# Performance work log

Measured on AMD Instinct MI355X. Metric: run time of the kernel, lower is better.

The kernel has to match this reference:

```python
import jax, jax.numpy as jnp
import numpy as np

N_NODES = 100000
N_EDGES = 3200000
N_GRAPHS = 512


def setup_inputs() -> dict:
    key = jax.random.key(0)
    k1, k2, k3, k4, k5 = jax.random.split(key, 5)
    x = jax.random.normal(k1, (N_NODES, 5), dtype=jnp.float32)
    edge_index = jax.random.randint(k2, (2, N_EDGES), 0, N_NODES, dtype=jnp.int64)
    batch = jnp.sort(jax.random.randint(k3, (N_NODES,), 0, N_GRAPHS, dtype=jnp.int64))
    W1 = jax.random.normal(k4, (5, 16), dtype=jnp.float32) * (1.0 / np.sqrt(5.0))
    b1 = jnp.zeros((16,), dtype=jnp.float32)
    W2 = jax.random.normal(k5, (16, 16), dtype=jnp.float32) * 0.25
    b2 = jnp.zeros((16,), dtype=jnp.float32)
    return {"x": x, "edge_index": edge_index, "batch": batch,
            "W1": W1, "b1": b1, "W2": W2, "b2": b2}


def _gcn_conv(x, src, dst, norm, W, b, n_nodes):
    # PyG GCNConv: h = X W; out_i = sum_{j->i} norm_ij * h_j + b
    h = x @ W                                   # [N, out]
    msgs = h[src] * norm[:, None]               # gather + scale  [E_tot, out]
    out = jax.ops.segment_sum(msgs, dst, num_segments=n_nodes)
    return out + b


def reference(x, edge_index, batch, W1, b1, W2, b2):
    n = x.shape[0]
    # add self-loops (GCNConv default)
    loops = jnp.arange(n, dtype=edge_index.dtype)
    src = jnp.concatenate([edge_index[0], loops])
    dst = jnp.concatenate([edge_index[1], loops])
    # symmetric normalization: deg computed on destination nodes
    deg = jax.ops.segment_sum(jnp.ones_like(src, dtype=x.dtype), dst, num_segments=n)
    dinv = jnp.where(deg > 0, jax.lax.rsqrt(deg), 0.0)
    norm = dinv[src] * dinv[dst]                # [E_tot]

    h = jax.nn.relu(_gcn_conv(x, src, dst, norm, W1, b1, n))
    h = jax.nn.relu(_gcn_conv(h, src, dst, norm, W2, b2, n))

    # global mean pool over graphs in the batch
    sums = jax.ops.segment_sum(h, batch, num_segments=N_GRAPHS)
    cnts = jax.ops.segment_sum(jnp.ones((n,), dtype=h.dtype), batch, num_segments=N_GRAPHS)
    return sums / jnp.maximum(cnts, 1.0)[:, None]
```

## Files before the change

kernel.cpp:

```cpp
#include <hip/hip_runtime.h>

#define N_NODES  100000
#define N_EDGES  3200000
#define N_GRAPHS 512
#define F_IN     5
#define F_HID    16

#define PBLK   512
#define CHUNK  4096
#define NBLK   ((N_EDGES + CHUNK - 1) / CHUNK)
#define BKT_NODES 256
#define NBKT ((N_NODES + BKT_NODES - 1) / BKT_NODES)
#define HPAD   512
#define CAP    10240
#define PN     64
#define NPB    ((N_NODES + PN - 1) / PN)


__device__ inline unsigned short f2bf(float f) {
    unsigned u = __float_as_uint(f);
    return (unsigned short)((u + 0x7fffu + ((u >> 16) & 1u)) >> 16);
}
__device__ inline float bf2f(unsigned short h) {
    return __uint_as_float(((unsigned)h) << 16);
}
__device__ inline void unpack16(uint4 r0, uint4 r1, float* f) {
    f[0]  = bf2f((unsigned short)r0.x); f[1]  = bf2f((unsigned short)(r0.x >> 16));
    f[2]  = bf2f((unsigned short)r0.y); f[3]  = bf2f((unsigned short)(r0.y >> 16));
    f[4]  = bf2f((unsigned short)r0.z); f[5]  = bf2f((unsigned short)(r0.z >> 16));
    f[6]  = bf2f((unsigned short)r0.w); f[7]  = bf2f((unsigned short)(r0.w >> 16));
    f[8]  = bf2f((unsigned short)r1.x); f[9]  = bf2f((unsigned short)(r1.x >> 16));
    f[10] = bf2f((unsigned short)r1.y); f[11] = bf2f((unsigned short)(r1.y >> 16));
    f[12] = bf2f((unsigned short)r1.z); f[13] = bf2f((unsigned short)(r1.z >> 16));
    f[14] = bf2f((unsigned short)r1.w); f[15] = bf2f((unsigned short)(r1.w >> 16));
}

template <int NW>
__device__ inline int block_incl_scan(int v, int t, int* wsum) {
    int lane = t & 63, wave = t >> 6;
    int x = v;
#pragma unroll
    for (int o = 1; o < 64; o <<= 1) {
        int y = __shfl_up(x, o, 64);
        if (lane >= o) x += y;
    }
    if (lane == 63) wsum[wave] = x;
    __syncthreads();
    if (t < 64) {
        int w = (t < NW) ? wsum[t] : 0;
#pragma unroll
        for (int o = 1; o < NW; o <<= 1) {
            int y = __shfl_up(w, o, 64);
            if (t >= o) w += y;
        }
        if (t < NW) wsum[t] = w;
    }
    __syncthreads();
    return x + (wave ? wsum[wave - 1] : 0);
}


__global__ __launch_bounds__(256) void k_zero(float* __restrict__ out,
                                              float* __restrict__ cnt) {
    int i = blockIdx.x * 256 + threadIdx.x;
    if (i < N_GRAPHS * F_HID) out[i] = 0.0f;
    if (i < N_GRAPHS) cnt[i] = 0.0f;
}

__global__ __launch_bounds__(PBLK) void k_count(const int* __restrict__ dst,
                                                const int* __restrict__ batch,
                                                int* __restrict__ H,
                                                int* __restrict__ Hc,
                                                float* __restrict__ cnt) {
    __shared__ int hist[HPAD];
    __shared__ int bcnt[8];
    __shared__ int g0s;
    int t = threadIdx.x, blk = blockIdx.x;
    int chunk0 = blk * CHUNK;
    int n4 = min(CHUNK, N_EDGES - chunk0) >> 2;
    hist[t] = 0;
    if (t < 8) bcnt[t] = 0;
    if (t == 0 && blk < NBKT) {
        int nb = blk * BKT_NODES;
        g0s = batch[nb < N_NODES ? nb : N_NODES - 1];
    }
    __syncthreads();
    const int4* d4 = (const int4*)(dst + chunk0);
#pragma unroll
    for (int i = 0; i < CHUNK / 4 / PBLK; i++) {
        int k = t + i * PBLK;
        if (k < n4) {
            int4 d = d4[k];
            atomicAdd(&hist[d.x >> 8], 1);
            atomicAdd(&hist[d.y >> 8], 1);
            atomicAdd(&hist[d.z >> 8], 1);
            atomicAdd(&hist[d.w >> 8], 1);
        }
    }
    if (blk < NBKT && t < BKT_NODES) {
        int i2 = blk * BKT_NODES + t;
        if (i2 < N_NODES) {
            int g = batch[i2];
            int l = g - g0s;
            if (l >= 0 && l < 8) atomicAdd(&bcnt[l], 1);
            else atomicAdd(&cnt[g], 1.0f);
        }
    }
    __syncthreads();
    int v = hist[t];
    H[blk * HPAD + t] = v;
    Hc[blk * HPAD + t] = v;
    if (blk < NBKT && t < 8 && bcnt[t] > 0) atomicAdd(&cnt[g0s + t], (float)bcnt[t]);
}

__global__ __launch_bounds__(256) void k_scan(int* __restrict__ H,
                                              int* __restrict__ cnt_b) {
    __shared__ int wsum[8];
    int b = blockIdx.x, t = threadIdx.x;
    int v[4];
    int s = 0;
#pragma unroll
    for (int i = 0; i < 4; i++) {
        int pos = t * 4 + i;
        v[i] = (pos < NBLK) ? H[pos * HPAD + b] : 0;
        s += v[i];
    }
    int incl = block_incl_scan<4>(s, t, wsum);
    int run = incl - s;
#pragma unroll
    for (int i = 0; i < 4; i++) {
        int pos = t * 4 + i;
        if (pos < NBLK) H[pos * HPAD + b] = run;
        run += v[i];
    }
    if (t == 255) cnt_b[b] = incl;
}

__global__ __launch_bounds__(PBLK) void k_scatter(const int* __restrict__ src,
                                                  const int* __restrict__ dst,
                                                  const int* __restrict__ H,
                                                  const int* __restrict__ Hc,
                                                  unsigned* __restrict__ packed) {
    __shared__ int scn[HPAD];
    __shared__ int rnk[HPAD];
    __shared__ int base[HPAD];
    __shared__ int wsum[8];
    __shared__ unsigned pkd[CHUNK];
    __shared__ unsigned short bkt[CHUNK];
    int t = threadIdx.x, blk = blockIdx.x;
    int chunk0 = blk * CHUNK;
    int n = min(CHUNK, N_EDGES - chunk0);
    int n4 = n >> 2;
    base[t] = H[blk * HPAD + t];
    int v = Hc[blk * HPAD + t];
    int incl = block_incl_scan<8>(v, t, wsum);
    int excl = incl - v;
    scn[t] = excl;
    rnk[t] = excl;
    __syncthreads();
    const int4* s4 = (const int4*)(src + chunk0);
    const int4* d4 = (const int4*)(dst + chunk0);
#pragma unroll
    for (int i = 0; i < CHUNK / 4 / PBLK; i++) {
        int k = t + i * PBLK;
        if (k < n4) {
            int4 s = s4[k], d = d4[k];
            int b0 = d.x >> 8, b1 = d.y >> 8, b2 = d.z >> 8, b3 = d.w >> 8;
            int r0 = atomicAdd(&rnk[b0], 1);
            pkd[r0] = ((unsigned)s.x << 8) | (unsigned)(d.x & 255);
            bkt[r0] = (unsigned short)b0;
            int r1 = atomicAdd(&rnk[b1], 1);
            pkd[r1] = ((unsigned)s.y << 8) | (unsigned)(d.y & 255);
            bkt[r1] = (unsigned short)b1;
            int r2 = atomicAdd(&rnk[b2], 1);
            pkd[r2] = ((unsigned)s.z << 8) | (unsigned)(d.z & 255);
            bkt[r2] = (unsigned short)b2;
            int r3 = atomicAdd(&rnk[b3], 1);
            pkd[r3] = ((unsigned)s.w << 8) | (unsigned)(d.w & 255);
            bkt[r3] = (unsigned short)b3;
        }
    }
    __syncthreads();
    for (int p = t; p < n; p += PBLK) {
        int b = bkt[p];
        packed[(size_t)b * CAP + base[b] + (p - scn[b])] = pkd[p];
    }
}

__global__ __launch_bounds__(512) void k_csr(const int* __restrict__ cnt_b,
                                             const unsigned* __restrict__ packed,
                                             const float* __restrict__ x,
                                             const float* __restrict__ W1,
                                             int2* __restrict__ rowbc,
                                             int* __restrict__ col,
                                             float* __restrict__ dinv,
                                             unsigned short* __restrict__ pb) {
    __shared__ int hist[BKT_NODES];
    __shared__ int beg[BKT_NODES];
    __shared__ int rnk2[BKT_NODES];
    __shared__ int wsum[8];
    __shared__ float w1[F_IN * F_HID];
    __shared__ unsigned pkd[CAP];
    __shared__ int tots;
    int b = blockIdx.x, t = threadIdx.x;
    int gbase = b * CAP;
    if (t < BKT_NODES) hist[t] = 0;
    if (t == 0) tots = min(cnt_b[b], CAP);
    if (t >= 512 - F_IN * F_HID) w1[t - (512 - F_IN * F_HID)] = W1[t - (512 - F_IN * F_HID)];
    __syncthreads();
    int tot = tots;
    const unsigned* pk = packed + (size_t)b * CAP;
    for (int k = t; k < tot; k += 512) {
        unsigned u = pk[k];
        pkd[k] = u;
        atomicAdd(&hist[u & 255], 1);
    }
    __syncthreads();
    int v = (t < BKT_NODES) ? hist[t] : 0;
    int incl = block_incl_scan<8>(v, t, wsum);
    if (t < BKT_NODES) { beg[t] = incl - v; rnk2[t] = incl - v; }
    __syncthreads();
    for (int e = t; e < tot; e += 512) {
        unsigned w = pkd[e];
        int r = atomicAdd(&rnk2[w & 255], 1);
        col[gbase + r] = (int)(w >> 8);
    }
    if (t < BKT_NODES) {
        int node = b * BKT_NODES + t;
        if (node < N_NODES) {
            rowbc[node] = make_int2(gbase + beg[t], v);
            float di = rsqrtf((float)(1 + v));
            dinv[node] = di;
            float xi[F_IN];
#pragma unroll
            for (int k = 0; k < F_IN; k++) xi[k] = x[node * F_IN + k];
            unsigned pkk[8];
#pragma unroll
            for (int q = 0; q < 8; q++) {
                float h0 = 0.0f, h1 = 0.0f;
#pragma unroll
                for (int k = 0; k < F_IN; k++) {
                    h0 += xi[k] * w1[k * F_HID + 2 * q];
                    h1 += xi[k] * w1[k * F_HID + 2 * q + 1];
                }
                pkk[q] = (unsigned)f2bf(h0 * di) | ((unsigned)f2bf(h1 * di) << 16);
            }
            uint4* d4 = (uint4*)(pb + (size_t)node * F_HID);
            d4[0] = make_uint4(pkk[0], pkk[1], pkk[2], pkk[3]);
            d4[1] = make_uint4(pkk[4], pkk[5], pkk[6], pkk[7]);
        }
    }
}

__global__ __launch_bounds__(256) void k_pull1(const int2* __restrict__ rowbc,
                                               const int* __restrict__ col,
                                               const unsigned short* __restrict__ pb,
                                               const float* __restrict__ dinv,
                                               const float* __restrict__ W2,
                                               const float* __restrict__ b1,
                                               unsigned short* __restrict__ pb2) {
    __shared__ float w2[F_HID * F_HID];
    __shared__ float b1s[F_HID];
    int t = threadIdx.x;
    w2[t] = W2[t];
    if (t < F_HID) b1s[t] = b1[t];
    __syncthreads();
    int nl = t >> 2, q = t & 3;
    int node = blockIdx.x * PN + nl;
    const uint4* pb16 = (const uint4*)pb;
    float f[F_HID];
#pragma unroll
    for (int c = 0; c < F_HID; c++) f[c] = 0.0f;
    if (node < N_NODES) {
        int2 rc = rowbc[node];
        if (q == 0) unpack16(pb16[2 * node], pb16[2 * node + 1], f);
        for (int i = q; i < rc.y; i += 4) {
            int s = col[rc.x + i];
            uint4 r0 = pb16[2 * s], r1 = pb16[2 * s + 1];
            float g[F_HID];
            unpack16(r0, r1, g);
#pragma unroll
            for (int c = 0; c < F_HID; c++) f[c] += g[c];
        }
    }
#pragma unroll
    for (int c = 0; c < F_HID; c++) {
        f[c] += __shfl_xor(f[c], 1, 64);
        f[c] += __shfl_xor(f[c], 2, 64);
    }
    if (node < N_NODES) {
        float di = dinv[node];
        float h[F_HID];
#pragma unroll
        for (int c = 0; c < F_HID; c++)
            h[c] = fmaxf(di * f[c] + b1s[c], 0.0f);
        float m0 = 0.0f, m1 = 0.0f, m2 = 0.0f, m3 = 0.0f;
#pragma unroll
        for (int c = 0; c < F_HID; c++) {
            float4 wv = *(const float4*)&w2[c * F_HID + 4 * q];
            m0 += h[c] * wv.x; m1 += h[c] * wv.y; m2 += h[c] * wv.z; m3 += h[c] * wv.w;
        }
        unsigned p0 = (unsigned)f2bf(m0 * di) | ((unsigned)f2bf(m1 * di) << 16);
        unsigned p1 = (unsigned)f2bf(m2 * di) | ((unsigned)f2bf(m3 * di) << 16);
        *(uint2*)(pb2 + (size_t)node * F_HID + 4 * q) = make_uint2(p0, p1);
    }
}

__global__ __launch_bounds__(256) void k_pull2(const int2* __restrict__ rowbc,
                                               const int* __restrict__ col,
                                               const unsigned short* __restrict__ pb,
                                               const float* __restrict__ dinv,
                                               const int* __restrict__ batch,
                                               const float* __restrict__ b2,
                                               const float* __restrict__ cnt,
                                               float* __restrict__ out) {
    __shared__ float b2s[F_HID];
    __shared__ float hbuf[PN][F_HID + 1];
    __shared__ int bl[PN];
    int t = threadIdx.x;
    if (t < F_HID) b2s[t] = b2[t];
    if (t < PN) {
        int nn = blockIdx.x * PN + t;
        bl[t] = (nn < N_NODES) ? batch[nn] : -1;
    }
    __syncthreads();
    int nl = t >> 2, q = t & 3;
    int node = blockIdx.x * PN + nl;
    const uint4* pb16 = (const uint4*)pb;
    float f[F_HID];
#pragma unroll
    for (int c = 0; c < F_HID; c++) f[c] = 0.0f;
    if (node < N_NODES) {
        int2 rc = rowbc[node];
        if (q == 0) unpack16(pb16[2 * node], pb16[2 * node + 1], f);
        for (int i = q; i < rc.y; i += 4) {
            int s = col[rc.x + i];
            uint4 r0 = pb16[2 * s], r1 = pb16[2 * s + 1];
            float g[F_HID];
            unpack16(r0, r1, g);
#pragma unroll
            for (int c = 0; c < F_HID; c++) f[c] += g[c];
        }
    }
#pragma unroll
    for (int c = 0; c < F_HID; c++) {
        f[c] += __shfl_xor(f[c], 1, 64);
        f[c] += __shfl_xor(f[c], 2, 64);
    }
    if (node < N_NODES && q == 0) {
        float di = dinv[node];
#pragma unroll
        for (int c = 0; c < F_HID; c++)
            hbuf[nl][c] = fmaxf(di * f[c] + b2s[c], 0.0f);
    }
    __syncthreads();
    if (t < 8 * F_HID) {
        int l = t >> 4, ch = t & 15;
        int g = bl[0] + l;
        if (g < N_GRAPHS) {
            float s = 0.0f;
            int m = 0;
            for (int n0 = 0; n0 < PN; n0++) {
                int n = (n0 + (ch << 2)) & (PN - 1);
                if (bl[n] == g) { s += hbuf[n][ch]; m++; }
            }
            if (m > 0) atomicAdd(&out[g * F_HID + ch], s / cnt[g]);
        }
    }
}


extern "C" void kernel_launch(void* const* d_in, const int* in_sizes, int n_in,
                              void* d_out, int out_size, void* d_ws, size_t ws_size,
                              hipStream_t stream) {
    const float* x     = (const float*)d_in[0];
    const int*   ei    = (const int*)d_in[1];
    const int*   batch = (const int*)d_in[2];
    const float* W1    = (const float*)d_in[3];
    const float* b1    = (const float*)d_in[4];
    const float* W2    = (const float*)d_in[5];
    const float* b2    = (const float*)d_in[6];
    float* out = (float*)d_out;

    int*            H      = (int*)d_ws;
    int*            Hc     = H + (size_t)NBLK * HPAD;
    int*            cnt_b  = Hc + (size_t)NBLK * HPAD;
    unsigned*       packed = (unsigned*)(cnt_b + 512);
    int2*           rowbc  = (int2*)(packed + (size_t)NBKT * CAP);
    int*            col    = (int*)(rowbc + N_NODES);
    float*          dinv   = (float*)(col + (size_t)NBKT * CAP);
    unsigned short* pb_a   = (unsigned short*)(dinv + N_NODES);
    unsigned short* pb_b   = pb_a + (size_t)N_NODES * F_HID;
    float*          cnt    = (float*)(pb_b + (size_t)N_NODES * F_HID);

    const int* src = ei;
    const int* dst = ei + N_EDGES;

    k_zero   <<<(N_GRAPHS * F_HID + 255) / 256, 256, 0, stream>>>(out, cnt);
    k_count  <<<NBLK, PBLK, 0, stream>>>(dst, batch, H, Hc, cnt);
    k_scan   <<<NBKT, 256, 0, stream>>>(H, cnt_b);
    k_scatter<<<NBLK, PBLK, 0, stream>>>(src, dst, H, Hc, packed);
    k_csr    <<<NBKT, 512, 0, stream>>>(cnt_b, packed, x, W1, rowbc, col, dinv, pb_a);
    k_pull1  <<<NPB, 256, 0, stream>>>(rowbc, col, pb_a, dinv, W2, b1, pb_b);
    k_pull2  <<<NPB, 256, 0, stream>>>(rowbc, col, pb_b, dinv, batch, b2, cnt, out);
}
```

Measured before the change: 196.7 us.

## Reuse histogram atomic ranks instead of recomputing them in scatter and CSR

The count kernel now stores the per-edge rank returned by its shared-memory histogram atomic into a ushort global buffer. The scatter kernel reads these ranks and no longer repeats the atomics. The CSR kernel likewise keeps its histogram ranks in registers for the column write instead of running a second atomic pass. The cost removed is duplicated LDS atomic contention; in exchange there is an extra 6.4 MB write and read of ranks through global memory.

```diff
diff --git a/kernel.cpp b/kernel.cpp
--- a/kernel.cpp
+++ b/kernel.cpp
@@ -13,6 +13,7 @@
 #define NBKT ((N_NODES + BKT_NODES - 1) / BKT_NODES)
 #define HPAD   512
 #define CAP    10240
+#define CPT    (CAP / 512)
 #define PN     64
 #define NPB    ((N_NODES + PN - 1) / PN)
 
@@ -71,6 +72,7 @@
                                                 const int* __restrict__ batch,
                                                 int* __restrict__ H,
                                                 int* __restrict__ Hc,
+                                                unsigned short* __restrict__ rnk_e,
                                                 float* __restrict__ cnt) {
     __shared__ int hist[HPAD];
     __shared__ int bcnt[8];
@@ -86,15 +88,18 @@
     }
     __syncthreads();
     const int4* d4 = (const int4*)(dst + chunk0);
+    ushort4* r4 = (ushort4*)(rnk_e + chunk0);
 #pragma unroll
     for (int i = 0; i < CHUNK / 4 / PBLK; i++) {
         int k = t + i * PBLK;
         if (k < n4) {
             int4 d = d4[k];
-            atomicAdd(&hist[d.x >> 8], 1);
-            atomicAdd(&hist[d.y >> 8], 1);
-            atomicAdd(&hist[d.z >> 8], 1);
-            atomicAdd(&hist[d.w >> 8], 1);
+            ushort4 rr;
+            rr.x = (unsigned short)atomicAdd(&hist[d.x >> 8], 1);
+            rr.y = (unsigned short)atomicAdd(&hist[d.y >> 8], 1);
+            rr.z = (unsigned short)atomicAdd(&hist[d.z >> 8], 1);
+            rr.w = (unsigned short)atomicAdd(&hist[d.w >> 8], 1);
+            r4[k] = rr;
         }
     }
     if (blk < NBKT && t < BKT_NODES) {
@@ -140,9 +145,9 @@
                                                   const int* __restrict__ dst,
                                                   const int* __restrict__ H,
                                                   const int* __restrict__ Hc,
+                                                  const unsigned short* __restrict__ rnk_e,
                                                   unsigned* __restrict__ packed) {
     __shared__ int scn[HPAD];
-    __shared__ int rnk[HPAD];
     __shared__ int base[HPAD];
     __shared__ int wsum[8];
     __shared__ unsigned pkd[CHUNK];
@@ -154,30 +159,30 @@
     base[t] = H[blk * HPAD + t];
     int v = Hc[blk * HPAD + t];
     int incl = block_incl_scan<8>(v, t, wsum);
-    int excl = incl - v;
-    scn[t] = excl;
-    rnk[t] = excl;
+    scn[t] = incl - v;
     __syncthreads();
     const int4* s4 = (const int4*)(src + chunk0);
     const int4* d4 = (const int4*)(dst + chunk0);
+    const ushort4* r4 = (const ushort4*)(rnk_e + chunk0);
 #pragma unroll
     for (int i = 0; i < CHUNK / 4 / PBLK; i++) {
         int k = t + i * PBLK;
         if (k < n4) {
             int4 s = s4[k], d = d4[k];
+            ushort4 r = r4[k];
             int b0 = d.x >> 8, b1 = d.y >> 8, b2 = d.z >> 8, b3 = d.w >> 8;
-            int r0 = atomicAdd(&rnk[b0], 1);
-            pkd[r0] = ((unsigned)s.x << 8) | (unsigned)(d.x & 255);
-            bkt[r0] = (unsigned short)b0;
-            int r1 = atomicAdd(&rnk[b1], 1);
-            pkd[r1] = ((unsigned)s.y << 8) | (unsigned)(d.y & 255);
-            bkt[r1] = (unsigned short)b1;
-            int r2 = atomicAdd(&rnk[b2], 1);
-            pkd[r2] = ((unsigned)s.z << 8) | (unsigned)(d.z & 255);
-            bkt[r2] = (unsigned short)b2;
-            int r3 = atomicAdd(&rnk[b3], 1);
-            pkd[r3] = ((unsigned)s.w << 8) | (unsigned)(d.w & 255);
-            bkt[r3] = (unsigned short)b3;
+            int p0 = scn[b0] + r.x;
+            pkd[p0] = ((unsigned)s.x << 8) | (unsigned)(d.x & 255);
+            bkt[p0] = (unsigned short)b0;
+            int p1 = scn[b1] + r.y;
+            pkd[p1] = ((unsigned)s.y << 8) | (unsigned)(d.y & 255);
+            bkt[p1] = (unsigned short)b1;
+            int p2 = scn[b2] + r.z;
+            pkd[p2] = ((unsigned)s.z << 8) | (unsigned)(d.z & 255);
+            bkt[p2] = (unsigned short)b2;
+            int p3 = scn[b3] + r.w;
+            pkd[p3] = ((unsigned)s.w << 8) | (unsigned)(d.w & 255);
+            bkt[p3] = (unsigned short)b3;
         }
     }
     __syncthreads();
@@ -197,7 +202,6 @@
                                              unsigned short* __restrict__ pb) {
     __shared__ int hist[BKT_NODES];
     __shared__ int beg[BKT_NODES];
-    __shared__ int rnk2[BKT_NODES];
     __shared__ int wsum[8];
     __shared__ float w1[F_IN * F_HID];
     __shared__ unsigned pkd[CAP];
@@ -210,20 +214,28 @@
     __syncthreads();
     int tot = tots;
     const unsigned* pk = packed + (size_t)b * CAP;
-    for (int k = t; k < tot; k += 512) {
-        unsigned u = pk[k];
-        pkd[k] = u;
-        atomicAdd(&hist[u & 255], 1);
+    int r2[CPT];
+#pragma unroll
+    for (int i = 0; i < CPT; i++) {
+        int k = t + i * 512;
+        if (k < tot) {
+            unsigned u = pk[k];
+            pkd[k] = u;
+            r2[i] = atomicAdd(&hist[u & 255], 1);
+        }
     }
     __syncthreads();
     int v = (t < BKT_NODES) ? hist[t] : 0;
     int incl = block_incl_scan<8>(v, t, wsum);
-    if (t < BKT_NODES) { beg[t] = incl - v; rnk2[t] = incl - v; }
-    __syncthreads();
-    for (int e = t; e < tot; e += 512) {
-        unsigned w = pkd[e];
-        int r = atomicAdd(&rnk2[w & 255], 1);
-        col[gbase + r] = (int)(w >> 8);
+    if (t < BKT_NODES) beg[t] = incl - v;
+    __syncthreads();
+#pragma unroll
+    for (int i = 0; i < CPT; i++) {
+        int k = t + i * 512;
+        if (k < tot) {
+            unsigned w = pkd[k];
+            col[gbase + beg[w & 255] + r2[i]] = (int)(w >> 8);
+        }
     }
     if (t < BKT_NODES) {
         int node = b * BKT_NODES + t;
@@ -385,7 +397,8 @@
     int*            H      = (int*)d_ws;
     int*            Hc     = H + (size_t)NBLK * HPAD;
     int*            cnt_b  = Hc + (size_t)NBLK * HPAD;
-    unsigned*       packed = (unsigned*)(cnt_b + 512);
+    unsigned short* rnk_e  = (unsigned short*)(cnt_b + 512);
+    unsigned*       packed = (unsigned*)(rnk_e + (size_t)N_EDGES);
     int2*           rowbc  = (int2*)(packed + (size_t)NBKT * CAP);
     int*            col    = (int*)(rowbc + N_NODES);
     float*          dinv   = (float*)(col + (size_t)NBKT * CAP);
@@ -397,9 +410,9 @@
     const int* dst = ei + N_EDGES;
 
     k_zero   <<<(N_GRAPHS * F_HID + 255) / 256, 256, 0, stream>>>(out, cnt);
-    k_count  <<<NBLK, PBLK, 0, stream>>>(dst, batch, H, Hc, cnt);
+    k_count  <<<NBLK, PBLK, 0, stream>>>(dst, batch, H, Hc, rnk_e, cnt);
     k_scan   <<<NBKT, 256, 0, stream>>>(H, cnt_b);
-    k_scatter<<<NBLK, PBLK, 0, stream>>>(src, dst, H, Hc, packed);
+    k_scatter<<<NBLK, PBLK, 0, stream>>>(src, dst, H, Hc, rnk_e, packed);
     k_csr    <<<NBKT, 512, 0, stream>>>(cnt_b, packed, x, W1, rowbc, col, dinv, pb_a);
     k_pull1  <<<NPB, 256, 0, stream>>>(rowbc, col, pb_a, dinv, W2, b1, pb_b);
     k_pull2  <<<NPB, 256, 0, stream>>>(rowbc, col, pb_b, dinv, batch, b2, cnt, out);
```

Result: no change. 197.8 us (+0.6%).
